# Performance work log

Hardware: AMD Instinct MI355X
Metric: run time of the kernel (lower is better)

## Reference

```python
import jax, jax.numpy as jnp
import numpy as np

V_EN = 50000; V_FR = 50000; D = 256; B = 64; S = 64; NEG = 8192; PAD = 0


def setup_inputs() -> dict:
    key = jax.random.key(0)
    k = jax.random.split(key, 8)
    zs = jax.random.normal(k[0], (B, S, D), dtype=jnp.float32) * 0.1
    x_en = jax.random.randint(k[1], (B, S), 1, V_EN)  # avoid pad row 0
    x_fr = jax.random.randint(k[2], (B, S), 1, V_FR)
    en_mask = jnp.ones((B, S), dtype=jnp.float32)
    fr_mask = jnp.ones((B, S), dtype=jnp.float32)
    W_en = jax.random.normal(k[3], (V_EN, D), dtype=jnp.float32) * 0.05
    W_en = W_en.at[PAD].set(0.0)  # padding_idx row is zero
    W_fr = jax.random.normal(k[4], (V_FR, D), dtype=jnp.float32) * 0.05
    W_fr = W_fr.at[PAD].set(0.0)
    # Host-side CSS sampling, mirroring the torch module's numpy/multinomial step.
    rng = np.random.default_rng(0)
    pos_en = np.unique(np.asarray(x_en))
    neg_en = rng.choice(np.setdiff1d(np.arange(V_EN), pos_en), NEG, replace=False)
    kappa_en = jnp.float32((V_EN - pos_en.shape[0]) / NEG)
    pos_fr = np.unique(np.asarray(x_fr))
    neg_fr = rng.choice(np.setdiff1d(np.arange(V_FR), pos_fr), NEG, replace=False)
    kappa_fr = jnp.float32((V_FR - pos_fr.shape[0]) / NEG)
    return {
        "zs": zs, "x_en": x_en, "x_fr": x_fr,
        "en_mask": en_mask, "fr_mask": fr_mask,
        "W_en": W_en, "W_fr": W_fr,
        "pos_en": jnp.asarray(pos_en), "neg_en": jnp.asarray(neg_en),
        "pos_fr": jnp.asarray(pos_fr), "neg_fr": jnp.asarray(neg_fr),
        "kappa_en": kappa_en, "kappa_fr": kappa_fr,
    }


def _css_denom(zs, W, pos_idx, neg_idx, kappa):
    # zs: [B,S,D]; pos/neg embeddings: [P,D]/[N,D] -> denom [B,S]
    pos_e = W[pos_idx]
    neg_e = W[neg_idx]
    pos_score = jnp.exp(jnp.einsum("bsd,pd->bsp", zs, pos_e)).sum(-1)
    neg_score = kappa * jnp.exp(jnp.einsum("bsd,nd->bsn", zs, neg_e)).sum(-1)
    return pos_score + neg_score


def reference(zs, x_en, x_fr, en_mask, fr_mask, W_en, W_fr,
              pos_en, neg_en, pos_fr, neg_fr, kappa_en, kappa_fr):
    # --- English CSS: per-token score ---
    be_en = W_en[x_en]                                   # [B,S,D]
    en_batch = jnp.exp((zs * be_en).sum(-1))             # [B,S]
    en_probs = en_batch / _css_denom(zs, W_en, pos_en, neg_en, kappa_en)
    # --- French CSS: alignment score against every en position ---
    be_fr = W_fr[x_fr]                                   # [B,Sf,D]
    fr_batch = jnp.exp(jnp.einsum("bfd,bsd->bfs", be_fr, zs))  # [B,Sf,S]
    fr_denom = _css_denom(zs, W_fr, pos_fr, neg_fr, kappa_fr)  # [B,S]
    fr_probs = fr_batch / fr_denom[:, None, :]
    en_rec_loss = (jnp.log(en_probs) * en_mask).sum(axis=1)            # [B]
    fr_rec_loss = (jnp.log(fr_probs.sum(axis=2)) * fr_mask).sum(axis=1)  # [B]
    return en_rec_loss, fr_rec_loss
```

## Files before the change

kernel.cpp:

```cpp
#include <hip/hip_runtime.h>

#define DDIM 256
#define NTOK 4096
#define NEGN 8192
#define TM 64
#define TN 64
#define LDT 40

typedef __attribute__((ext_vector_type(8))) short bf16x8;
typedef __attribute__((ext_vector_type(4))) float f32x4;

__device__ inline unsigned short f2bf(float f) {
    unsigned int u = __float_as_uint(f);
    unsigned int r = u + 0x7FFFu + ((u >> 16) & 1u);
    return (unsigned short)(r >> 16);
}

__device__ inline void gl_lds16(const unsigned short* g, unsigned short* l) {
    __builtin_amdgcn_global_load_lds(
        reinterpret_cast<__attribute__((address_space(1))) unsigned int*>(
            reinterpret_cast<uintptr_t>(g)),
        reinterpret_cast<__attribute__((address_space(3))) unsigned int*>(
            reinterpret_cast<uintptr_t>(l)),
        16, 0, 0);
}

template<int CTRL>
__device__ inline float dpp_add(float x) {
    int v = __builtin_amdgcn_update_dpp(0, __float_as_int(x), CTRL, 0xF, 0xF, false);
    return x + __int_as_float(v);
}
__device__ inline float red16(float x) {
    x = dpp_add<0xB1>(x);
    x = dpp_add<0x4E>(x);
    x = dpp_add<0x141>(x);
    x = dpp_add<0x140>(x);
    return x;
}

__global__ void gather_kernel(
    const float* __restrict__ zs,
    const float* __restrict__ W_en, const float* __restrict__ W_fr,
    const int* __restrict__ pos_en, const int* __restrict__ neg_en,
    const int* __restrict__ pos_fr, const int* __restrict__ neg_fr,
    const int* __restrict__ x_en,
    const float* __restrict__ kappa_en, const float* __restrict__ kappa_fr,
    unsigned short* __restrict__ z_bf,
    unsigned short* __restrict__ E_en, unsigned short* __restrict__ E_fr,
    float* __restrict__ w_en, float* __restrict__ w_fr,
    float* __restrict__ en_score,
    int Pe, int Pf, int Lpe, int Lpf)
{
    int row  = blockIdx.x * 4 + (threadIdx.x >> 6);
    int lane = threadIdx.x & 63;
    const float* src = nullptr;
    unsigned short* dst = nullptr;
    bool zero = false;

    if (row < NTOK) {
        src = zs + (size_t)row * DDIM;
        dst = z_bf + (size_t)row * DDIM;
    } else if (row < NTOK + Lpe) {
        int j = row - NTOK;
        int Le = Pe + NEGN;
        int idx = 0;
        if (j < Pe)      idx = pos_en[j];
        else if (j < Le) idx = neg_en[j - Pe];
        else             zero = true;
        src = W_en + (size_t)idx * DDIM;
        dst = E_en + (size_t)j * DDIM;
        if (lane == 0) w_en[j] = (j < Pe) ? 1.0f : (j < Le ? kappa_en[0] : 0.0f);
    } else if (row < NTOK + Lpe + Lpf) {
        int j = row - NTOK - Lpe;
        int Lf = Pf + NEGN;
        int idx = 0;
        if (j < Pf)      idx = pos_fr[j];
        else if (j < Lf) idx = neg_fr[j - Pf];
        else             zero = true;
        src = W_fr + (size_t)idx * DDIM;
        dst = E_fr + (size_t)j * DDIM;
        if (lane == 0) w_fr[j] = (j < Pf) ? 1.0f : (j < Lf ? kappa_fr[0] : 0.0f);
    } else if (row < NTOK + Lpe + Lpf + NTOK) {
        int j = row - NTOK - Lpe - Lpf;
        int idx = x_en[j];
        float4 z = *(const float4*)(zs   + (size_t)j   * DDIM + lane * 4);
        float4 w = *(const float4*)(W_en + (size_t)idx * DDIM + lane * 4);
        float s = z.x * w.x + z.y * w.y + z.z * w.z + z.w * w.w;
        #pragma unroll
        for (int m = 32; m; m >>= 1) s += __shfl_xor(s, m);
        if (lane == 0) en_score[j] = s;
        return;
    } else {
        return;
    }

    int d = lane * 4;
    float4 v;
    if (zero) { v.x = v.y = v.z = v.w = 0.0f; }
    else      { v = *(const float4*)(src + d); }
    ushort4 o;
    o.x = f2bf(v.x); o.y = f2bf(v.y); o.z = f2bf(v.z); o.w = f2bf(v.w);
    *(ushort4*)(dst + d) = o;
}

__global__ __launch_bounds__(256, 2) void expsum_stream(
    const unsigned short* __restrict__ A,
    const unsigned short* __restrict__ E,
    const float* __restrict__ wts,
    float* __restrict__ out_en, float* __restrict__ out_fr,
    int Lpe, int NT)
{
    __shared__ __align__(16) unsigned short Bs[2][128 * 32];

    int fid = blockIdx.y * 32 + blockIdx.x;
    int xcd = fid & 7;
    int r   = fid >> 3;
    int yb  = xcd * 2 + (r & 1);
    int xb  = r >> 1;

    int t    = threadIdx.x;
    int lane = t & 63;
    int wave = t >> 6;
    int col  = lane & 15;
    int quad = lane >> 4;
    int wm   = wave & 1;
    int wn   = wave >> 1;

    bf16x8 afr[4][8];
    {
        const unsigned short* Ap =
            A + ((size_t)(xb * 128 + wm * 64 + col)) * DDIM + quad * 8;
        #pragma unroll
        for (int i = 0; i < 4; i++)
            #pragma unroll
            for (int c = 0; c < 8; c++)
                afr[i][c] = *(const bf16x8*)(Ap + (size_t)i * 16 * DDIM + c * 32);
    }

    float sums[4][4];
    #pragma unroll
    for (int i = 0; i < 4; i++)
        #pragma unroll
        for (int rr = 0; rr < 4; rr++) sums[i][rr] = 0.0f;
    float* curout = out_en;
    int outrow = xb * 128 + wm * 64;

    int p = 0;
    {
        const unsigned short* g0 = E + (size_t)(yb * 128 + 32 * wave + col) * DDIM + quad * 8;
        gl_lds16(g0,             &Bs[0][wave * 1024]);
        gl_lds16(g0 + 16 * DDIM, &Bs[0][wave * 1024 + 512]);
    }

    for (int tl = yb; tl < NT; tl += 16) {
        int nb = tl * 128;
        float* o = (nb >= Lpe) ? out_fr : out_en;
        if (o != curout) {
            if (col == 0) {
                #pragma unroll
                for (int i = 0; i < 4; i++)
                    #pragma unroll
                    for (int rr = 0; rr < 4; rr++)
                        atomicAdd(curout + outrow + 16 * i + quad * 4 + rr, sums[i][rr]);
            }
            #pragma unroll
            for (int i = 0; i < 4; i++)
                #pragma unroll
                for (int rr = 0; rr < 4; rr++) sums[i][rr] = 0.0f;
            curout = o;
        }

        float wj[4];
        #pragma unroll
        for (int j = 0; j < 4; j++)
            wj[j] = wts[nb + wn * 64 + 16 * j + col];

        f32x4 acc[4][4];
        #pragma unroll
        for (int i = 0; i < 4; i++)
            #pragma unroll
            for (int j = 0; j < 4; j++)
                acc[i][j] = (f32x4){0.f, 0.f, 0.f, 0.f};

        #pragma unroll
        for (int k8 = 0; k8 < 8; k8++) {
            __syncthreads();
            if (k8 < 7) {
                const unsigned short* g0 =
                    E + (size_t)(nb + 32 * wave + col) * DDIM + (k8 + 1) * 32 + quad * 8;
                gl_lds16(g0,             &Bs[p ^ 1][wave * 1024]);
                gl_lds16(g0 + 16 * DDIM, &Bs[p ^ 1][wave * 1024 + 512]);
            } else if (tl + 16 < NT) {
                const unsigned short* g0 =
                    E + (size_t)((tl + 16) * 128 + 32 * wave + col) * DDIM + quad * 8;
                gl_lds16(g0,             &Bs[p ^ 1][wave * 1024]);
                gl_lds16(g0 + 16 * DDIM, &Bs[p ^ 1][wave * 1024 + 512]);
            }
            bf16x8 bfv[4];
            #pragma unroll
            for (int j = 0; j < 4; j++)
                bfv[j] = *(const bf16x8*)(&Bs[p][(wn * 4 + j) * 512 + quad * 128 + col * 8]);
            #pragma unroll
            for (int j = 0; j < 4; j++)
                #pragma unroll
                for (int i = 0; i < 4; i++)
                    acc[i][j] = __builtin_amdgcn_mfma_f32_16x16x32_bf16(
                        afr[i][k8], bfv[j], acc[i][j], 0, 0, 0);
            p ^= 1;
        }

        #pragma unroll
        for (int i = 0; i < 4; i++)
            #pragma unroll
            for (int rr = 0; rr < 4; rr++) {
                float s = wj[0] * __expf(acc[i][0][rr]) + wj[1] * __expf(acc[i][1][rr])
                        + wj[2] * __expf(acc[i][2][rr]) + wj[3] * __expf(acc[i][3][rr]);
                sums[i][rr] += red16(s);
            }
    }

    if (col == 0) {
        #pragma unroll
        for (int i = 0; i < 4; i++)
            #pragma unroll
            for (int rr = 0; rr < 4; rr++)
                atomicAdd(curout + outrow + 16 * i + quad * 4 + rr, sums[i][rr]);
    }
}

__global__ __launch_bounds__(256) void expsum_gemm64_loss(
    const float* __restrict__ W_fr,
    const int* __restrict__ x_fr,
    const unsigned short* __restrict__ Bm,
    const float* __restrict__ denom_fr,
    const float* __restrict__ denom_en,
    const float* __restrict__ en_score,
    const float* __restrict__ en_mask,
    const float* __restrict__ fr_mask,
    float* __restrict__ outloss)
{
    __shared__ __align__(16) unsigned short lda[TM * LDT];
    __shared__ __align__(16) unsigned short ldb[TN * LDT];
    __shared__ float tbuf[64];

    int batch = blockIdx.x;
    const unsigned short* Bb = Bm + (size_t)batch * TN * DDIM;

    int t      = threadIdx.x;
    int srow   = t >> 2;
    int schunk = t & 3;
    int lane   = t & 63;
    int wave   = t >> 6;
    int col    = lane & 15;
    int quad   = lane >> 4;

    int aidx = x_fr[batch * 64 + srow];
    const float* Arow = W_fr + (size_t)aidx * DDIM;

    f32x4 acc0 = {0.f,0.f,0.f,0.f};
    f32x4 acc1 = {0.f,0.f,0.f,0.f};
    f32x4 acc2 = {0.f,0.f,0.f,0.f};
    f32x4 acc3 = {0.f,0.f,0.f,0.f};

    for (int kk = 0; kk < DDIM; kk += 32) {
        float4 f0 = *(const float4*)(Arow + kk + schunk * 8);
        float4 f1 = *(const float4*)(Arow + kk + schunk * 8 + 4);
        uint4 bv = *(const uint4*)(Bb + (size_t)srow * DDIM + kk + schunk * 8);
        ushort4 ua; ua.x = f2bf(f0.x); ua.y = f2bf(f0.y); ua.z = f2bf(f0.z); ua.w = f2bf(f0.w);
        ushort4 ub; ub.x = f2bf(f1.x); ub.y = f2bf(f1.y); ub.z = f2bf(f1.z); ub.w = f2bf(f1.w);
        __syncthreads();
        *(ushort4*)(lda + srow * LDT + schunk * 8)     = ua;
        *(ushort4*)(lda + srow * LDT + schunk * 8 + 4) = ub;
        *(uint4*)(ldb + srow * LDT + schunk * 8) = bv;
        __syncthreads();

        bf16x8 af = *(const bf16x8*)(lda + (wave * 16 + col) * LDT + quad * 8);
        bf16x8 b0 = *(const bf16x8*)(ldb + ( 0 + col) * LDT + quad * 8);
        bf16x8 b1 = *(const bf16x8*)(ldb + (16 + col) * LDT + quad * 8);
        bf16x8 b2 = *(const bf16x8*)(ldb + (32 + col) * LDT + quad * 8);
        bf16x8 b3 = *(const bf16x8*)(ldb + (48 + col) * LDT + quad * 8);
        acc0 = __builtin_amdgcn_mfma_f32_16x16x32_bf16(af, b0, acc0, 0, 0, 0);
        acc1 = __builtin_amdgcn_mfma_f32_16x16x32_bf16(af, b1, acc1, 0, 0, 0);
        acc2 = __builtin_amdgcn_mfma_f32_16x16x32_bf16(af, b2, acc2, 0, 0, 0);
        acc3 = __builtin_amdgcn_mfma_f32_16x16x32_bf16(af, b3, acc3, 0, 0, 0);
    }

    const float* db = denom_fr + batch * 64;
    float w0 = 1.0f / db[ 0 + col];
    float w1 = 1.0f / db[16 + col];
    float w2 = 1.0f / db[32 + col];
    float w3 = 1.0f / db[48 + col];

    float tot0 = w0 * __expf(acc0.x) + w1 * __expf(acc1.x) + w2 * __expf(acc2.x) + w3 * __expf(acc3.x);
    float tot1 = w0 * __expf(acc0.y) + w1 * __expf(acc1.y) + w2 * __expf(acc2.y) + w3 * __expf(acc3.y);
    float tot2 = w0 * __expf(acc0.z) + w1 * __expf(acc1.z) + w2 * __expf(acc2.z) + w3 * __expf(acc3.z);
    float tot3 = w0 * __expf(acc0.w) + w1 * __expf(acc1.w) + w2 * __expf(acc2.w) + w3 * __expf(acc3.w);

    #pragma unroll
    for (int m = 1; m < 16; m <<= 1) {
        tot0 += __shfl_xor(tot0, m);
        tot1 += __shfl_xor(tot1, m);
        tot2 += __shfl_xor(tot2, m);
        tot3 += __shfl_xor(tot3, m);
    }
    if (col == 0) {
        int base = wave * 16 + quad * 4;
        tbuf[base + 0] = tot0; tbuf[base + 1] = tot1;
        tbuf[base + 2] = tot2; tbuf[base + 3] = tot3;
    }
    __syncthreads();

    if (t < 64) {
        int i = batch * 64 + t;
        float a = (en_score[i] - __logf(denom_en[i])) * en_mask[i];
        float c = __logf(tbuf[t]) * fr_mask[i];
        #pragma unroll
        for (int m = 32; m; m >>= 1) { a += __shfl_xor(a, m); c += __shfl_xor(c, m); }
        if (t == 0) { outloss[batch] = a; outloss[64 + batch] = c; }
    }
}

extern "C" void kernel_launch(void* const* d_in, const int* in_sizes, int n_in,
                              void* d_out, int out_size, void* d_ws, size_t ws_size,
                              hipStream_t stream)
{
    const float* zs       = (const float*)d_in[0];
    const int*   x_en     = (const int*)d_in[1];
    const int*   x_fr     = (const int*)d_in[2];
    const float* en_mask  = (const float*)d_in[3];
    const float* fr_mask  = (const float*)d_in[4];
    const float* W_en     = (const float*)d_in[5];
    const float* W_fr     = (const float*)d_in[6];
    const int*   pos_en   = (const int*)d_in[7];
    const int*   neg_en   = (const int*)d_in[8];
    const int*   pos_fr   = (const int*)d_in[9];
    const int*   neg_fr   = (const int*)d_in[10];
    const float* kappa_en = (const float*)d_in[11];
    const float* kappa_fr = (const float*)d_in[12];

    int Pe  = in_sizes[7];
    int Pf  = in_sizes[9];
    int Lpe = (Pe + NEGN + 127) & ~127;
    int Lpf = (Pf + NEGN + 127) & ~127;
    int Ltot = Lpe + Lpf;
    int NT   = Ltot / 128;

    char* w = (char*)d_ws;
    float* denom_en = (float*)w; w += NTOK * 4;
    float* denom_fr = (float*)w; w += NTOK * 4;
    float* en_score = (float*)w; w += NTOK * 4;
    float* w_all    = (float*)w; w += (size_t)Ltot * 4;
    unsigned short* z_bf  = (unsigned short*)w; w += (size_t)NTOK * DDIM * 2;
    unsigned short* E_all = (unsigned short*)w; w += (size_t)Ltot * DDIM * 2;

    hipMemsetAsync(denom_en, 0, (size_t)NTOK * 2 * 4, stream);

    int totrows = NTOK + Lpe + Lpf + NTOK;
    gather_kernel<<<(totrows + 3) / 4, 256, 0, stream>>>(
        zs, W_en, W_fr, pos_en, neg_en, pos_fr, neg_fr, x_en,
        kappa_en, kappa_fr, z_bf, E_all, E_all + (size_t)Lpe * DDIM,
        w_all, w_all + Lpe, en_score, Pe, Pf, Lpe, Lpf);

    expsum_stream<<<dim3(32, 16), 256, 0, stream>>>(
        z_bf, E_all, w_all, denom_en, denom_fr, Lpe, NT);

    expsum_gemm64_loss<<<64, 256, 0, stream>>>(
        W_fr, x_fr, z_bf, denom_fr, denom_en, en_score, en_mask, fr_mask,
        (float*)d_out);
}
```

Before: 218.8 us.

## Give each wave private LDS buffers and drop block barriers in expsum stream

After: 243.4 us. +11.3%, slower.

```diff
diff --git a/kernel.cpp b/kernel.cpp
--- a/kernel.cpp
+++ b/kernel.cpp
@@ -23,6 +23,12 @@
         reinterpret_cast<__attribute__((address_space(3))) unsigned int*>(
             reinterpret_cast<uintptr_t>(l)),
         16, 0, 0);
+}
+
+__device__ inline void dma_chunk(const unsigned short* gbase, unsigned short* ldsbase) {
+    #pragma unroll
+    for (int s = 0; s < 4; s++)
+        gl_lds16(gbase + (size_t)s * 16 * DDIM, ldsbase + s * 512);
 }
 
 template<int CTRL>
@@ -49,6 +55,7 @@
     unsigned short* __restrict__ E_en, unsigned short* __restrict__ E_fr,
     float* __restrict__ w_en, float* __restrict__ w_fr,
     float* __restrict__ en_score,
+    float* __restrict__ denom_en, float* __restrict__ denom_fr,
     int Pe, int Pf, int Lpe, int Lpf)
 {
     int row  = blockIdx.x * 4 + (threadIdx.x >> 6);
@@ -60,6 +67,7 @@
     if (row < NTOK) {
         src = zs + (size_t)row * DDIM;
         dst = z_bf + (size_t)row * DDIM;
+        if (lane == 0) { denom_en[row] = 0.0f; denom_fr[row] = 0.0f; }
     } else if (row < NTOK + Lpe) {
         int j = row - NTOK;
         int Le = Pe + NEGN;
@@ -110,7 +118,7 @@
     float* __restrict__ out_en, float* __restrict__ out_fr,
     int Lpe, int NT)
 {
-    __shared__ __align__(16) unsigned short Bs[2][128 * 32];
+    __shared__ __align__(16) unsigned short Bs[4][2][2048];
 
     int fid = blockIdx.y * 32 + blockIdx.x;
     int xcd = fid & 7;
@@ -145,15 +153,22 @@
     float* curout = out_en;
     int outrow = xb * 128 + wm * 64;
 
+    unsigned short* lds0 = &Bs[wave][0][0];
+    unsigned short* lds1 = &Bs[wave][1][0];
+
+    dma_chunk(E + (size_t)(yb * 128 + wn * 64 + col) * DDIM + quad * 8, lds0);
+
     int p = 0;
-    {
-        const unsigned short* g0 = E + (size_t)(yb * 128 + 32 * wave + col) * DDIM + quad * 8;
-        gl_lds16(g0,             &Bs[0][wave * 1024]);
-        gl_lds16(g0 + 16 * DDIM, &Bs[0][wave * 1024 + 512]);
-    }
-
     for (int tl = yb; tl < NT; tl += 16) {
         int nb = tl * 128;
+        const unsigned short* gtile =
+            E + (size_t)(nb + wn * 64 + col) * DDIM + quad * 8;
+
+        float wj[4];
+        #pragma unroll
+        for (int j = 0; j < 4; j++)
+            wj[j] = wts[nb + wn * 64 + 16 * j + col];
+
         float* o = (nb >= Lpe) ? out_fr : out_en;
         if (o != curout) {
             if (col == 0) {
@@ -170,11 +185,6 @@
             curout = o;
         }
 
-        float wj[4];
-        #pragma unroll
-        for (int j = 0; j < 4; j++)
-            wj[j] = wts[nb + wn * 64 + 16 * j + col];
-
         f32x4 acc[4][4];
         #pragma unroll
         for (int i = 0; i < 4; i++)
@@ -184,22 +194,22 @@
 
         #pragma unroll
         for (int k8 = 0; k8 < 8; k8++) {
-            __syncthreads();
+            unsigned short* cbuf = p ? lds1 : lds0;
+            unsigned short* nbuf = p ? lds0 : lds1;
             if (k8 < 7) {
-                const unsigned short* g0 =
-                    E + (size_t)(nb + 32 * wave + col) * DDIM + (k8 + 1) * 32 + quad * 8;
-                gl_lds16(g0,             &Bs[p ^ 1][wave * 1024]);
-                gl_lds16(g0 + 16 * DDIM, &Bs[p ^ 1][wave * 1024 + 512]);
+                dma_chunk(gtile + (k8 + 1) * 32, nbuf);
+                asm volatile("s_waitcnt vmcnt(4)" ::: "memory");
             } else if (tl + 16 < NT) {
-                const unsigned short* g0 =
-                    E + (size_t)((tl + 16) * 128 + 32 * wave + col) * DDIM + quad * 8;
-                gl_lds16(g0,             &Bs[p ^ 1][wave * 1024]);
-                gl_lds16(g0 + 16 * DDIM, &Bs[p ^ 1][wave * 1024 + 512]);
+                dma_chunk(E + (size_t)((tl + 16) * 128 + wn * 64 + col) * DDIM + quad * 8,
+                          nbuf);
+                asm volatile("s_waitcnt vmcnt(4)" ::: "memory");
+            } else {
+                asm volatile("s_waitcnt vmcnt(0)" ::: "memory");
             }
             bf16x8 bfv[4];
             #pragma unroll
             for (int j = 0; j < 4; j++)
-                bfv[j] = *(const bf16x8*)(&Bs[p][(wn * 4 + j) * 512 + quad * 128 + col * 8]);
+                bfv[j] = *(const bf16x8*)(cbuf + j * 512 + quad * 128 + col * 8);
             #pragma unroll
             for (int j = 0; j < 4; j++)
                 #pragma unroll
@@ -353,13 +363,11 @@
     unsigned short* z_bf  = (unsigned short*)w; w += (size_t)NTOK * DDIM * 2;
     unsigned short* E_all = (unsigned short*)w; w += (size_t)Ltot * DDIM * 2;
 
-    hipMemsetAsync(denom_en, 0, (size_t)NTOK * 2 * 4, stream);
-
     int totrows = NTOK + Lpe + Lpf + NTOK;
     gather_kernel<<<(totrows + 3) / 4, 256, 0, stream>>>(
         zs, W_en, W_fr, pos_en, neg_en, pos_fr, neg_fr, x_en,
         kappa_en, kappa_fr, z_bf, E_all, E_all + (size_t)Lpe * DDIM,
-        w_all, w_all + Lpe, en_score, Pe, Pf, Lpe, Lpf);
+        w_all, w_all + Lpe, en_score, denom_en, denom_fr, Pe, Pf, Lpe, Lpf);
 
     expsum_stream<<<dim3(32, 16), 256, 0, stream>>>(
         z_bf, E_all, w_all, denom_en, denom_fr, Lpe, NT);
```

## Deepen LDS prefetch to four buffers with vmcnt waits and fold memset into gather

Applied to the files above, without the earlier changes.

After: 208.8 us. 1.05x faster.

```diff
diff --git a/kernel.cpp b/kernel.cpp
--- a/kernel.cpp
+++ b/kernel.cpp
@@ -24,6 +24,11 @@
             reinterpret_cast<uintptr_t>(l)),
         16, 0, 0);
 }
+
+__device__ inline void wait_vmcnt4() { asm volatile("s_waitcnt vmcnt(4)" ::: "memory"); }
+__device__ inline void wait_vmcnt2() { asm volatile("s_waitcnt vmcnt(2)" ::: "memory"); }
+__device__ inline void wait_vmcnt0() { asm volatile("s_waitcnt vmcnt(0)" ::: "memory"); }
+__device__ inline void raw_barrier() { asm volatile("s_barrier" ::: "memory"); }
 
 template<int CTRL>
 __device__ inline float dpp_add(float x) {
@@ -49,6 +54,7 @@
     unsigned short* __restrict__ E_en, unsigned short* __restrict__ E_fr,
     float* __restrict__ w_en, float* __restrict__ w_fr,
     float* __restrict__ en_score,
+    float* __restrict__ denom_en, float* __restrict__ denom_fr,
     int Pe, int Pf, int Lpe, int Lpf)
 {
     int row  = blockIdx.x * 4 + (threadIdx.x >> 6);
@@ -60,6 +66,7 @@
     if (row < NTOK) {
         src = zs + (size_t)row * DDIM;
         dst = z_bf + (size_t)row * DDIM;
+        if (lane == 0) { denom_en[row] = 0.0f; denom_fr[row] = 0.0f; }
     } else if (row < NTOK + Lpe) {
         int j = row - NTOK;
         int Le = Pe + NEGN;
@@ -110,7 +117,7 @@
     float* __restrict__ out_en, float* __restrict__ out_fr,
     int Lpe, int NT)
 {
-    __shared__ __align__(16) unsigned short Bs[2][128 * 32];
+    __shared__ __align__(16) unsigned short Bs[4][4096];
 
     int fid = blockIdx.y * 32 + blockIdx.x;
     int xcd = fid & 7;
@@ -145,15 +152,27 @@
     float* curout = out_en;
     int outrow = xb * 128 + wm * 64;
 
-    int p = 0;
+    int ntiles = (NT - yb + 15) >> 4;
+
     {
-        const unsigned short* g0 = E + (size_t)(yb * 128 + 32 * wave + col) * DDIM + quad * 8;
-        gl_lds16(g0,             &Bs[0][wave * 1024]);
-        gl_lds16(g0 + 16 * DDIM, &Bs[0][wave * 1024 + 512]);
-    }
-
-    for (int tl = yb; tl < NT; tl += 16) {
+        const unsigned short* g0 =
+            E + (size_t)(yb * 128 + 32 * wave + col) * DDIM + quad * 8;
+        gl_lds16(g0,                 &Bs[0][wave * 1024]);
+        gl_lds16(g0 + 16 * DDIM,     &Bs[0][wave * 1024 + 512]);
+        gl_lds16(g0 + 32,            &Bs[1][wave * 1024]);
+        gl_lds16(g0 + 16 * DDIM + 32,&Bs[1][wave * 1024 + 512]);
+    }
+
+    for (int s = 0; s < ntiles; s++) {
+        int tl = yb + (s << 4);
         int nb = tl * 128;
+        bool last = (s == ntiles - 1);
+
+        float wj[4];
+        #pragma unroll
+        for (int j = 0; j < 4; j++)
+            wj[j] = wts[nb + wn * 64 + 16 * j + col];
+
         float* o = (nb >= Lpe) ? out_fr : out_en;
         if (o != curout) {
             if (col == 0) {
@@ -170,11 +189,6 @@
             curout = o;
         }
 
-        float wj[4];
-        #pragma unroll
-        for (int j = 0; j < 4; j++)
-            wj[j] = wts[nb + wn * 64 + 16 * j + col];
-
         f32x4 acc[4][4];
         #pragma unroll
         for (int i = 0; i < 4; i++)
@@ -184,38 +198,43 @@
 
         #pragma unroll
         for (int k8 = 0; k8 < 8; k8++) {
-            __syncthreads();
-            if (k8 < 7) {
-                const unsigned short* g0 =
-                    E + (size_t)(nb + 32 * wave + col) * DDIM + (k8 + 1) * 32 + quad * 8;
-                gl_lds16(g0,             &Bs[p ^ 1][wave * 1024]);
-                gl_lds16(g0 + 16 * DDIM, &Bs[p ^ 1][wave * 1024 + 512]);
-            } else if (tl + 16 < NT) {
-                const unsigned short* g0 =
-                    E + (size_t)((tl + 16) * 128 + 32 * wave + col) * DDIM + quad * 8;
-                gl_lds16(g0,             &Bs[p ^ 1][wave * 1024]);
-                gl_lds16(g0 + 16 * DDIM, &Bs[p ^ 1][wave * 1024 + 512]);
+            int rb = k8 & 3;
+            int rs = (k8 + 2) & 3;
+            if (!last || k8 < 6) {
+                int c2  = s * 8 + k8 + 2;
+                int tl2 = yb + ((c2 >> 3) << 4);
+                int kk2 = (c2 & 7) * 32;
+                const unsigned short* g =
+                    E + (size_t)(tl2 * 128 + 32 * wave + col) * DDIM + kk2 + quad * 8;
+                gl_lds16(g,             &Bs[rs][wave * 1024]);
+                gl_lds16(g + 16 * DDIM, &Bs[rs][wave * 1024 + 512]);
+                wait_vmcnt4();
+            } else if (k8 == 6) {
+                wait_vmcnt2();
+            } else {
+                wait_vmcnt0();
             }
+            raw_barrier();
+
             bf16x8 bfv[4];
             #pragma unroll
             for (int j = 0; j < 4; j++)
-                bfv[j] = *(const bf16x8*)(&Bs[p][(wn * 4 + j) * 512 + quad * 128 + col * 8]);
+                bfv[j] = *(const bf16x8*)(&Bs[rb][(wn * 4 + j) * 512 + quad * 128 + col * 8]);
             #pragma unroll
             for (int j = 0; j < 4; j++)
                 #pragma unroll
                 for (int i = 0; i < 4; i++)
                     acc[i][j] = __builtin_amdgcn_mfma_f32_16x16x32_bf16(
                         afr[i][k8], bfv[j], acc[i][j], 0, 0, 0);
-            p ^= 1;
         }
 
         #pragma unroll
         for (int i = 0; i < 4; i++)
             #pragma unroll
             for (int rr = 0; rr < 4; rr++) {
-                float s = wj[0] * __expf(acc[i][0][rr]) + wj[1] * __expf(acc[i][1][rr])
-                        + wj[2] * __expf(acc[i][2][rr]) + wj[3] * __expf(acc[i][3][rr]);
-                sums[i][rr] += red16(s);
+                float sv = wj[0] * __expf(acc[i][0][rr]) + wj[1] * __expf(acc[i][1][rr])
+                         + wj[2] * __expf(acc[i][2][rr]) + wj[3] * __expf(acc[i][3][rr]);
+                sums[i][rr] += red16(sv);
             }
     }
 
@@ -353,13 +372,11 @@
     unsigned short* z_bf  = (unsigned short*)w; w += (size_t)NTOK * DDIM * 2;
     unsigned short* E_all = (unsigned short*)w; w += (size_t)Ltot * DDIM * 2;
 
-    hipMemsetAsync(denom_en, 0, (size_t)NTOK * 2 * 4, stream);
-
     int totrows = NTOK + Lpe + Lpf + NTOK;
     gather_kernel<<<(totrows + 3) / 4, 256, 0, stream>>>(
         zs, W_en, W_fr, pos_en, neg_en, pos_fr, neg_fr, x_en,
         kappa_en, kappa_fr, z_bf, E_all, E_all + (size_t)Lpe * DDIM,
-        w_all, w_all + Lpe, en_score, Pe, Pf, Lpe, Lpf);
+        w_all, w_all + Lpe, en_score, denom_en, denom_fr, Pe, Pf, Lpe, Lpf);
 
     expsum_stream<<<dim3(32, 16), 256, 0, stream>>>(
         z_bf, E_all, w_all, denom_en, denom_fr, Lpe, NT);
```
